# Performance work log

Measured on AMD Instinct MI355X. Metric: run time of the kernel, lower is better.

Reference implementation:

```python
import jax, jax.numpy as jnp
import numpy as np
from jax import lax

WS = 8  # window size

def conv1x1(x, W, b=None):
    y = jnp.einsum('bchw,oc->bohw', x, W)
    if b is not None:
        y = y + b[None, :, None, None]
    return y

def conv2d(x, W, b=None, dilation=1, groups=1):
    p = dilation * (W.shape[-1] // 2)
    y = lax.conv_general_dilated(x, W, (1, 1), [(p, p), (p, p)],
                                 rhs_dilation=(dilation, dilation),
                                 feature_group_count=groups,
                                 dimension_numbers=('NCHW', 'OIHW', 'NCHW'))
    if b is not None:
        y = y + b[None, :, None, None]
    return y

def ln_cf(x, w, b, eps=1e-6):
    # channels_first LayerNorm over channel dim
    u = x.mean(1, keepdims=True)
    s = ((x - u) ** 2).mean(1, keepdims=True)
    return w[None, :, None, None] * ((x - u) / jnp.sqrt(s + eps)) + b[None, :, None, None]

def to_windows(x):
    # b c (h dh) (w dw) -> b (h w) (dh dw c)
    B, C, H, W = x.shape
    h, w = H // WS, W // WS
    return x.reshape(B, C, h, WS, w, WS).transpose(0, 2, 4, 3, 5, 1).reshape(B, h * w, WS * WS * C)

def from_windows(x, C, H, W):
    B = x.shape[0]
    h, w = H // WS, W // WS
    return x.reshape(B, h, w, WS, WS, C).transpose(0, 5, 1, 3, 2, 4).reshape(B, C, H, W)

def lrelu(x):
    return jnp.where(x >= 0, x, 0.1 * x)

def gelu(x):
    return jax.nn.gelu(x, approximate=False)  # torch exact GELU

def _forward(x, w_norm1, b_norm1, w_norm2, b_norm2,
             Wv, bv, Wq, bq, Wk, bk, dw1, dwb1, dw2, dwb2, Wo, bo,
             W_in, b_in, Wc, bc, ln_w, ln_b, Wm1, bm1, Wm2, bm2,
             Wca, bca, Wsa, bsa, Wffn_in, dw_ffn, Wffn_out):
    B, C, H, W = x.shape
    ws2 = WS * WS
    N = (H // WS) * (W // WS)
    embed = ws2 * C
    # ---------- CAMixer ----------
    v = conv1x1(x, Wv, bv)
    # MaskPre routing
    xin = lrelu(conv1x1(v, W_in, b_in))                 # (B, C/4, H, W)
    x_ = lrelu(ln_cf(conv1x1(v, Wc, bc), ln_w, ln_b))   # (B, C/4, H, W)
    ca = jax.nn.sigmoid(conv1x1(x_.mean((2, 3), keepdims=True), Wca, bca))  # (B,C,1,1)
    sa = jax.nn.sigmoid(conv2d(x_, Wsa, bsa))           # (B,1,H,W)
    xm = to_windows(xin.mean(1, keepdims=True))         # (B,N,ws2)
    var = jnp.var(xm, axis=-1, ddof=1)                  # (B,N) torch.var unbiased
    k_top = N // 2
    _, idx = lax.top_k(-var, k_top)                     # bottom-k variance windows
    mbin = jnp.ones((B, N), x.dtype).at[jnp.arange(B)[:, None], idx].set(0.0)
    mfeat = jnp.broadcast_to(mbin[:, :, None], (B, N, embed))
    mask = lrelu(mfeat @ Wm1.T + bm1) @ Wm2.T + bm2     # (B,N,embed)
    # windowed content-routed attention
    vs = v * sa
    v_w, vs_w, x_w = to_windows(v), to_windows(vs), to_windows(x)
    v1 = (v_w * mask).reshape(B * N, ws2, C)
    v2 = vs_w * (1.0 - mask)
    t = (x_w * mask).reshape(B * N, ws2, C)             # masked q/k tokens (q=k=x)
    q1 = t @ Wq.T + bq
    k1 = t @ Wk.T + bk
    attn = jax.nn.softmax(q1 @ k1.transpose(0, 2, 1), axis=-1)  # (B*N, ws2, ws2)
    f = (attn @ v1).reshape(B, N, embed)
    img = from_windows(f + v2, C, H, W)
    cs = conv2d(conv2d(img, dw1, dwb1, 1, C), dw2, dwb2, 2, C)  # depthwise 3x3 + dilated
    out = gelu(cs) * ca + img
    res = conv1x1(out, Wo, bo)
    # ---------- norm1 + gated FFN + norm2 ----------
    x = ln_cf(x + res, w_norm1, b_norm1)
    y = conv2d(conv1x1(x, Wffn_in), dw_ffn, None, 1, 2 * C)
    y1, y2 = jnp.split(y, 2, axis=1)
    res = conv1x1(gelu(y1) * y2, Wffn_out)
    return ln_cf(x + res, w_norm2, b_norm2)

def setup_inputs():
    key = jax.random.key(0)
    B, C, H, W = 4, 64, 256, 256
    embed = WS * WS * C
    ks = iter(jax.random.split(key, 40))
    r = lambda *s: jax.random.normal(next(ks), s, jnp.float32) * 0.1
    return dict(
        x=jax.random.normal(next(ks), (B, C, H, W), jnp.float32),
        w_norm1=jnp.ones((C,), jnp.float32), b_norm1=jnp.zeros((C,), jnp.float32),
        w_norm2=jnp.ones((C,), jnp.float32), b_norm2=jnp.zeros((C,), jnp.float32),
        Wv=r(C, C), bv=r(C), Wq=r(C, C), bq=r(C), Wk=r(C, C), bk=r(C),
        dw1=r(C, 1, 3, 3), dwb1=r(C), dw2=r(C, 1, 3, 3), dwb2=r(C),
        Wo=r(C, C), bo=r(C),
        W_in=r(C // 4, C), b_in=r(C // 4), Wc=r(C // 4, C), bc=r(C // 4),
        ln_w=jnp.ones((C // 4,), jnp.float32), ln_b=jnp.zeros((C // 4,), jnp.float32),
        Wm1=r(embed // 2, embed) * 0.2, bm1=r(embed // 2),
        Wm2=r(embed, embed // 2) * 0.2, bm2=r(embed),
        Wca=r(C, C // 4), bca=r(C), Wsa=r(1, C // 4, 3, 3), bsa=r(1),
        Wffn_in=r(2 * C, C), dw_ffn=r(2 * C, 1, 3, 3), Wffn_out=r(C, C),
    )

def reference(x, w_norm1, b_norm1, w_norm2, b_norm2,
              Wv, bv, Wq, bq, Wk, bk, dw1, dwb1, dw2, dwb2, Wo, bo,
              W_in, b_in, Wc, bc, ln_w, ln_b, Wm1, bm1, Wm2, bm2,
              Wca, bca, Wsa, bsa, Wffn_in, dw_ffn, Wffn_out):
    return _forward(x, w_norm1, b_norm1, w_norm2, b_norm2,
                    Wv, bv, Wq, bq, Wk, bk, dw1, dwb1, dw2, dwb2, Wo, bo,
                    W_in, b_in, Wc, bc, ln_w, ln_b, Wm1, bm1, Wm2, bm2,
                    Wca, bca, Wsa, bsa, Wffn_in, dw_ffn, Wffn_out)
```

## Files before the change

### kernel.cpp

```cpp
#include <hip/hip_runtime.h>
#include <hip/hip_bf16.h>

typedef __hip_bfloat16 bf16;
typedef __attribute__((ext_vector_type(8))) short short8v;
typedef __attribute__((ext_vector_type(4))) float f32x4;

#define DEV static __device__ __forceinline__

DEV float b2f(bf16 h){ return __bfloat162float(h); }
DEV float us2f(unsigned short u){ unsigned v=((unsigned)u)<<16; float f; __builtin_memcpy(&f,&v,4); return f; }
DEV short f2bs(float f){ bf16 h=__float2bfloat16(f); short s; __builtin_memcpy(&s,&h,2); return s; }
DEV unsigned pack2(float a, float b){ return ((unsigned)(unsigned short)f2bs(b)<<16)|(unsigned short)f2bs(a); }
DEV float lrelu(float x){ return x >= 0.f ? x : 0.1f*x; }
DEV float geluf(float x){ return 0.5f*x*(1.f + erff(x*0.70710678118654752440f)); }
DEV float sigmoidf(float x){ return 1.f/(1.f + expf(-x)); }


__global__ __launch_bounds__(256) void k_detect(const void* x, int* flag){
  __shared__ int cnt;
  if(threadIdx.x==0) cnt=0;
  __syncthreads();
  const unsigned short* up=(const unsigned short*)x;
  int c=0;
  for(int k=0;k<16;k++){
    unsigned short u=up[(threadIdx.x*16+k)*2];
    if(((u>>7)&0xFF)==0xFF) c++;
  }
  atomicAdd(&cnt,c);
  __syncthreads();
  if(threadIdx.x==0) flag[0] = (cnt>0) ? 1 : 0;
}

struct CvtArgs { const void* src[31]; int sz[31]; int off[31]; };
__global__ __launch_bounds__(256) void k_cvt(CvtArgs a, const int* fl, float* wbuf){
  int t=blockIdx.x; int n=a.sz[t]; const void* s=a.src[t]; float* d=wbuf+a.off[t];
  if(fl[0]){
    const float* sp=(const float*)s;
    for(int i=threadIdx.x;i<n;i+=256) d[i]=sp[i];
  } else {
    const bf16* sp=(const bf16*)s;
    for(int i=threadIdx.x;i<n;i+=256) d[i]=b2f(sp[i]);
  }
}

__global__ __launch_bounds__(256) void k_w2b6(const float* __restrict__ wq, const float* __restrict__ wk,
    const float* __restrict__ wo, const float* __restrict__ wfi, const float* __restrict__ wfo,
    const float* __restrict__ wv,
    short* __restrict__ Wqb, short* __restrict__ Wkb,
    short* __restrict__ Wob, short* __restrict__ Wfib, short* __restrict__ Wfob,
    short* __restrict__ Wvb){
  int i=blockIdx.x*256+threadIdx.x;
  if(i<4096){ Wqb[i]=f2bs(wq[i]); Wkb[i]=f2bs(wk[i]); Wob[i]=f2bs(wo[i]); Wfob[i]=f2bs(wfo[i]); Wvb[i]=f2bs(wv[i]); }
  if(i<8192) Wfib[i]=f2bs(wfi[i]);
}

__global__ __launch_bounds__(256) void k_wcomp(const float* __restrict__ W_in, const float* __restrict__ b_in,
    const float* __restrict__ Wc, const float* __restrict__ bc,
    const float* __restrict__ Wv, const float* __restrict__ bv,
    float* __restrict__ Wa, float* __restrict__ ba,
    float* __restrict__ Wb2, float* __restrict__ bb2){
  int t=threadIdx.x;
  #pragma unroll
  for(int ii=0;ii<4;ii++){
    int idx=t+ii*256;
    int i=idx>>6, c=idx&63;
    float sa=0.f, sb=0.f;
    for(int k=0;k<64;k++){
      float wv=Wv[k*64+c];
      sa+=W_in[i*64+k]*wv;
      sb+=Wc[i*64+k]*wv;
    }
    Wa[idx]=sa; Wb2[idx]=sb;
  }
  if(t<16){
    float sa=0.f, sb=0.f;
    for(int k=0;k<64;k++){ sa+=W_in[t*64+k]*bv[k]; sb+=Wc[t*64+k]*bv[k]; }
    ba[t]=sa+b_in[t]; bb2[t]=sb+bc[t];
  }
}

__global__ __launch_bounds__(256) void k_convv_mf(
    const void* __restrict__ in, const int* __restrict__ fl,
    const short* __restrict__ Wvb, const float* __restrict__ bv,
    unsigned short* __restrict__ vw){
  __shared__ short Ain[64*72];
  int tid=threadIdx.x;
  int g0=blockIdx.x*64; int b=g0>>16, p0=g0&65535;
  int c=tid>>2, q=tid&3;
  size_t base=(((size_t)(b*64+c))<<16) + p0;
  if(fl[0]){
    const float* ip=(const float*)in + base;
    #pragma unroll
    for(int j=0;j<4;j++){
      int po=q*16+j*4;
      float4 xv=*(const float4*)(ip+po);
      Ain[(po+0)*72+c]=f2bs(xv.x); Ain[(po+1)*72+c]=f2bs(xv.y);
      Ain[(po+2)*72+c]=f2bs(xv.z); Ain[(po+3)*72+c]=f2bs(xv.w);
    }
  } else {
    const unsigned short* ip=(const unsigned short*)in + base;
    #pragma unroll
    for(int j=0;j<4;j++){
      int po=q*16+j*4;
      uint2 u=*(const uint2*)(ip+po);
      Ain[(po+0)*72+c]=(short)(u.x&0xffff); Ain[(po+1)*72+c]=(short)(u.x>>16);
      Ain[(po+2)*72+c]=(short)(u.y&0xffff); Ain[(po+3)*72+c]=(short)(u.y>>16);
    }
  }
  __syncthreads();
  int lane=tid&63, wid=tid>>6;
  int lr=lane&15, lg=lane>>4;
  int pix0=wid*16;
  short8v bfrag[2];
  #pragma unroll
  for(int ks=0;ks<2;ks++) bfrag[ks]=*(const short8v*)&Ain[(pix0+lr)*72 + ks*32 + lg*8];
  int y=p0>>8;
  int xx=(p0&255)+pix0+lr;
  int n=((y>>3)<<5)|(xx>>3), tok=((y&7)<<3)|(xx&7);
  unsigned short* wp=vw + (((size_t)(b*1024+n))<<12) + tok;
  #pragma unroll
  for(int nt=0;nt<4;nt++){
    f32x4 acc;
    #pragma unroll
    for(int r=0;r<4;r++) acc[r]=bv[nt*16+lg*4+r];
    #pragma unroll
    for(int ks=0;ks<2;ks++){
      short8v afrag=*(const short8v*)(Wvb + (nt*16+lr)*64 + ks*32 + lg*8);
      acc=__builtin_amdgcn_mfma_f32_16x16x32_bf16(afrag,bfrag[ks],acc,0,0,0);
    }
    #pragma unroll
    for(int r=0;r<4;r++){
      int m=nt*16+lg*4+r;
      wp[(size_t)m*64]=(unsigned short)f2bs(acc[r]);
    }
  }
}

__global__ __launch_bounds__(256) void k_gemm_mf(
    const void* __restrict__ in, int in_f32,
    const short* __restrict__ Wb, const float* __restrict__ bias, int has_bias,
    void* __restrict__ out, int och, int out_bf16){
  __shared__ short Ain[64*72];
  int tid=threadIdx.x;
  int g0=blockIdx.x*64; int b=g0>>16, p0=g0&65535;
  int c=tid>>2, q=tid&3;
  size_t base=(((size_t)(b*64+c))<<16) + p0;
  if(in_f32){
    const float* ip=(const float*)in + base;
    #pragma unroll
    for(int j=0;j<4;j++){
      int po=q*16+j*4;
      float4 xv=*(const float4*)(ip+po);
      Ain[(po+0)*72+c]=f2bs(xv.x); Ain[(po+1)*72+c]=f2bs(xv.y);
      Ain[(po+2)*72+c]=f2bs(xv.z); Ain[(po+3)*72+c]=f2bs(xv.w);
    }
  } else {
    const unsigned short* ip=(const unsigned short*)in + base;
    #pragma unroll
    for(int j=0;j<4;j++){
      int po=q*16+j*4;
      uint2 u=*(const uint2*)(ip+po);
      Ain[(po+0)*72+c]=(short)(u.x&0xffff); Ain[(po+1)*72+c]=(short)(u.x>>16);
      Ain[(po+2)*72+c]=(short)(u.y&0xffff); Ain[(po+3)*72+c]=(short)(u.y>>16);
    }
  }
  __syncthreads();
  int lane=tid&63, wid=tid>>6;
  int lr=lane&15, lg=lane>>4;
  int pix0=wid*16;
  short8v bfrag[2];
  #pragma unroll
  for(int ks=0;ks<2;ks++) bfrag[ks]=*(const short8v*)&Ain[(pix0+lr)*72 + ks*32 + lg*8];
  int ntn=och>>4;
  for(int nt=0;nt<ntn;nt++){
    f32x4 acc;
    if(has_bias){
      #pragma unroll
      for(int r=0;r<4;r++) acc[r]=bias[nt*16+lg*4+r];
    } else {
      acc=(f32x4){0.f,0.f,0.f,0.f};
    }
    #pragma unroll
    for(int ks=0;ks<2;ks++){
      short8v afrag=*(const short8v*)(Wb + (nt*16+lr)*64 + ks*32 + lg*8);
      acc=__builtin_amdgcn_mfma_f32_16x16x32_bf16(afrag,bfrag[ks],acc,0,0,0);
    }
    if(out_bf16){
      unsigned short* op=(unsigned short*)out;
      #pragma unroll
      for(int r=0;r<4;r++){
        int m=nt*16+lg*4+r;
        op[(((size_t)(b*och+m))<<16) + p0 + pix0 + lr]=(unsigned short)f2bs(acc[r]);
      }
    } else {
      float* op=(float*)out;
      #pragma unroll
      for(int r=0;r<4;r++){
        int m=nt*16+lg*4+r;
        op[(((size_t)(b*och+m))<<16) + p0 + pix0 + lr]=acc[r];
      }
    }
  }
}

__global__ __launch_bounds__(256) void k_gemm_ln(
    const unsigned short* __restrict__ in,
    const short* __restrict__ Wb, const float* __restrict__ bias, int has_bias,
    const void* __restrict__ basex,
    const float* __restrict__ lnw, const float* __restrict__ lnb,
    void* __restrict__ out,
    const int* __restrict__ fl, int base_mode, int out_mode){
  __shared__ short Ain[64*72];
  int tid=threadIdx.x;
  int g0=blockIdx.x*64; int b=g0>>16, p0=g0&65535;
  int c=tid>>2, q=tid&3;
  {
    const unsigned short* ip=in + (((size_t)(b*64+c))<<16) + p0;
    #pragma unroll
    for(int j=0;j<4;j++){
      int po=q*16+j*4;
      uint2 u=*(const uint2*)(ip+po);
      Ain[(po+0)*72+c]=(short)(u.x&0xffff); Ain[(po+1)*72+c]=(short)(u.x>>16);
      Ain[(po+2)*72+c]=(short)(u.y&0xffff); Ain[(po+3)*72+c]=(short)(u.y>>16);
    }
  }
  __syncthreads();
  int lane=tid&63, wid=tid>>6;
  int lr=lane&15, lg=lane>>4;
  int pix0=wid*16;
  short8v bfrag[2];
  #pragma unroll
  for(int ks=0;ks<2;ks++) bfrag[ks]=*(const short8v*)&Ain[(pix0+lr)*72 + ks*32 + lg*8];
  float rl[16];
  #pragma unroll
  for(int nt=0;nt<4;nt++){
    f32x4 acc;
    if(has_bias){
      #pragma unroll
      for(int r=0;r<4;r++) acc[r]=bias[nt*16+lg*4+r];
    } else {
      acc=(f32x4){0.f,0.f,0.f,0.f};
    }
    #pragma unroll
    for(int ks=0;ks<2;ks++){
      short8v afrag=*(const short8v*)(Wb + (nt*16+lr)*64 + ks*32 + lg*8);
      acc=__builtin_amdgcn_mfma_f32_16x16x32_bf16(afrag,bfrag[ks],acc,0,0,0);
    }
    #pragma unroll
    for(int r=0;r<4;r++) rl[nt*4+r]=acc[r];
  }
  int pix=p0+pix0+lr;
  bool bf32 = (base_mode==1) || (base_mode==0 && fl[0]);
  if(bf32){
    const float* xp=(const float*)basex;
    #pragma unroll
    for(int nt=0;nt<4;nt++)
      #pragma unroll
      for(int r=0;r<4;r++)
        rl[nt*4+r]+=xp[(((size_t)(b*64+nt*16+lg*4+r))<<16)+pix];
  } else {
    const unsigned short* xp=(const unsigned short*)basex;
    #pragma unroll
    for(int nt=0;nt<4;nt++)
      #pragma unroll
      for(int r=0;r<4;r++)
        rl[nt*4+r]+=us2f(xp[(((size_t)(b*64+nt*16+lg*4+r))<<16)+pix]);
  }
  float s=0.f;
  #pragma unroll
  for(int i=0;i<16;i++) s+=rl[i];
  s+=__shfl_xor(s,16); s+=__shfl_xor(s,32);
  float mean=s*(1.f/64.f);
  float qv=0.f;
  #pragma unroll
  for(int i=0;i<16;i++){ float d=rl[i]-mean; qv+=d*d; }
  qv+=__shfl_xor(qv,16); qv+=__shfl_xor(qv,32);
  float inv=1.f/sqrtf(qv*(1.f/64.f)+1e-6f);
  bool of32 = (out_mode==1) || (out_mode==0 && fl[0]);
  if(of32){
    float* op=(float*)out;
    #pragma unroll
    for(int nt=0;nt<4;nt++)
      #pragma unroll
      for(int r=0;r<4;r++){
        int m=nt*16+lg*4+r;
        op[(((size_t)(b*64+m))<<16)+pix]=lnw[m]*((rl[nt*4+r]-mean)*inv)+lnb[m];
      }
  } else {
    unsigned short* op=(unsigned short*)out;
    #pragma unroll
    for(int nt=0;nt<4;nt++)
      #pragma unroll
      for(int r=0;r<4;r++){
        int m=nt*16+lg*4+r;
        op[(((size_t)(b*64+m))<<16)+pix]=(unsigned short)f2bs(lnw[m]*((rl[nt*4+r]-mean)*inv)+lnb[m]);
      }
  }
}

__global__ __launch_bounds__(256) void k_route(const void* __restrict__ x, const int* __restrict__ fl,
    const float* __restrict__ Wa, const float* __restrict__ ba,
    const float* __restrict__ Wb2, const float* __restrict__ bb2,
    const float* __restrict__ lnw, const float* __restrict__ lnb,
    float* __restrict__ x_, float* __restrict__ xm, float* __restrict__ capart){
  __shared__ float wA[1024], wB[1024], sba[16], sbb[16], slw[16], slb[16];
  __shared__ float sred[4][16];
  int tid=threadIdx.x;
  for(int i=tid;i<1024;i+=256){ wA[i]=Wa[i]; wB[i]=Wb2[i]; }
  if(tid<16){ sba[tid]=ba[tid]; sbb[tid]=bb2[tid]; slw[tid]=lnw[tid]; slb[tid]=lnb[tid]; }
  __syncthreads();
  int g=blockIdx.x*512+tid*2; int b=g>>16, p=g&65535;
  float2 aA[16], aB[16];
  #pragma unroll
  for(int i=0;i<16;i++){ aA[i]=make_float2(sba[i],sba[i]); aB[i]=make_float2(sbb[i],sbb[i]); }
  size_t base=(((size_t)b*64)<<16)+p;
  if(fl[0]){
    const float* vp=(const float*)x+base;
    for(int c=0;c<64;c++){
      float2 vv=*(const float2*)(vp+(((size_t)c)<<16));
      #pragma unroll
      for(int i=0;i<16;i++){
        float wa=wA[(i<<6)+c], wb=wB[(i<<6)+c];
        aA[i].x+=wa*vv.x; aA[i].y+=wa*vv.y;
        aB[i].x+=wb*vv.x; aB[i].y+=wb*vv.y;
      }
    }
  } else {
    const unsigned short* vp=(const unsigned short*)x+base;
    for(int c=0;c<64;c++){
      unsigned u=*(const unsigned*)(vp+(((size_t)c)<<16));
      float v0=us2f(u&0xffff), v1=us2f(u>>16);
      #pragma unroll
      for(int i=0;i<16;i++){
        float wa=wA[(i<<6)+c], wb=wB[(i<<6)+c];
        aA[i].x+=wa*v0; aA[i].y+=wa*v1;
        aB[i].x+=wb*v0; aB[i].y+=wb*v1;
      }
    }
  }
  float s0=0.f,s1=0.f;
  #pragma unroll
  for(int i=0;i<16;i++){ aA[i].x=lrelu(aA[i].x); aA[i].y=lrelu(aA[i].y); s0+=aA[i].x; s1+=aA[i].y; }
  float2 xmst; xmst.x=s0*(1.f/16.f); xmst.y=s1*(1.f/16.f);
  *(float2*)(xm+g)=xmst;
  float u0=0.f,u1=0.f;
  #pragma unroll
  for(int i=0;i<16;i++){ u0+=aB[i].x; u1+=aB[i].y; }
  u0*=(1.f/16.f); u1*=(1.f/16.f);
  float q0=0.f,q1=0.f;
  #pragma unroll
  for(int i=0;i<16;i++){ float d0=aB[i].x-u0, d1=aB[i].y-u1; q0+=d0*d0; q1+=d1*d1; }
  q0*=(1.f/16.f); q1*=(1.f/16.f);
  float i0=1.f/sqrtf(q0+1e-6f), i1=1.f/sqrtf(q1+1e-6f);
  float red[16];
  float* xp=x_+(((size_t)b*16)<<16)+p;
  #pragma unroll
  for(int i=0;i<16;i++){
    float xv0=lrelu(slw[i]*((aB[i].x-u0)*i0)+slb[i]);
    float xv1=lrelu(slw[i]*((aB[i].y-u1)*i1)+slb[i]);
    float2 st; st.x=xv0; st.y=xv1;
    *(float2*)(xp+(((size_t)i)<<16))=st;
    red[i]=xv0+xv1;
  }
  int lane=tid&63, wid=tid>>6;
  #pragma unroll
  for(int i=0;i<16;i++){
    float val=red[i];
    for(int m=32;m>0;m>>=1) val+=__shfl_xor(val,m);
    if(lane==0) sred[wid][i]=val;
  }
  __syncthreads();
  if(tid<16) capart[blockIdx.x*16+tid]=sred[0][tid]+sred[1][tid]+sred[2][tid]+sred[3][tid];
}

__global__ __launch_bounds__(256) void k_sa(const float* __restrict__ x_,
    const float* __restrict__ Wsa, const float* __restrict__ bsa, unsigned short* __restrict__ sa_w){
  __shared__ float w[144]; __shared__ float bb;
  int tid=threadIdx.x;
  if(tid<144) w[tid]=Wsa[tid];
  if(tid==0) bb=bsa[0];
  __syncthreads();
  int pix=blockIdx.x*256+tid; int b=pix>>16, p=pix&65535;
  int y=p>>8, xx=p&255;
  float acc=bb;
  #pragma unroll
  for(int i=0;i<16;i++){
    const float* pl=x_+(((size_t)(b*16+i))<<16);
    #pragma unroll
    for(int ky=0;ky<3;ky++){
      int yy=y+ky-1;
      if((unsigned)yy<256u){
        #pragma unroll
        for(int kx=0;kx<3;kx++){
          int x2=xx+kx-1;
          if((unsigned)x2<256u) acc+=pl[(yy<<8)+x2]*w[i*9+ky*3+kx];
        }
      }
    }
  }
  int n=((y>>3)<<5)|(xx>>3), tok=((y&7)<<3)|(xx&7);
  sa_w[(((size_t)(b<<10)+n)<<6)+tok]=(unsigned short)f2bs(sigmoidf(acc));
}

__global__ __launch_bounds__(64) void k_var(const float* __restrict__ xm, float* __restrict__ var){
  int blk=blockIdx.x, tid=threadIdx.x;
  int b=blk>>10, n=blk&1023;
  int pix=((n>>5)<<11) + ((n&31)<<3) + ((tid>>3)<<8) + (tid&7);
  float val=xm[(b<<16)+pix];
  float s=val;
  for(int m=32;m>0;m>>=1) s+=__shfl_xor(s,m);
  float mean=s*(1.f/64.f);
  float d=val-mean; float q=d*d;
  for(int m=32;m>0;m>>=1) q+=__shfl_xor(q,m);
  if(tid==0) var[blk]=q*(1.f/63.f);
}

__global__ __launch_bounds__(256) void k_rank(const float* __restrict__ var, float* __restrict__ mbin){
  __shared__ float va[1024];
  int bid=blockIdx.x; int b=bid>>2, seg=bid&3;
  int tid=threadIdx.x;
  for(int i=tid;i<1024;i+=256) va[i]=var[(b<<10)+i];
  __syncthreads();
  int n=seg*256+tid;
  float vn=va[n]; int r=0;
  for(int m=0;m<1024;m++){ float vm=va[m]; r += (vm<vn) || (vm==vn && m<n); }
  mbin[(b<<10)+n] = (r<512)?0.f:1.f;
}

__global__ __launch_bounds__(64) void k_hvec(const void* __restrict__ Wm1, const float* __restrict__ bm1,
    float* __restrict__ h0, float* __restrict__ h1, const int* __restrict__ fl){
  int j=blockIdx.x, tid=threadIdx.x;
  float s=0.f;
  if(fl[0]){
    const float* row=(const float*)Wm1+((size_t)j<<12);
    for(int k=tid;k<4096;k+=64) s+=row[k];
  } else {
    const bf16* row=(const bf16*)Wm1+((size_t)j<<12);
    for(int k=tid;k<4096;k+=64) s+=b2f(row[k]);
  }
  for(int m=32;m>0;m>>=1) s+=__shfl_xor(s,m);
  if(tid==0){ float bb=bm1[j]; h0[j]=lrelu(bb); h1[j]=lrelu(bb+s); }
}

__global__ __launch_bounds__(64) void k_mask(const void* __restrict__ Wm2, const float* __restrict__ bm2,
    const float* __restrict__ h0, const float* __restrict__ h1,
    float* __restrict__ m0, float* __restrict__ m1,
    float* __restrict__ m0T, float* __restrict__ m1T, const int* __restrict__ fl){
  int e=blockIdx.x, tid=threadIdx.x;
  float p0=0.f,p1=0.f;
  if(fl[0]){
    const float* row=(const float*)Wm2+((size_t)e<<11);
    for(int j=tid;j<2048;j+=64){ float w=row[j]; p0+=w*h0[j]; p1+=w*h1[j]; }
  } else {
    const bf16* row=(const bf16*)Wm2+((size_t)e<<11);
    for(int j=tid;j<2048;j+=64){ float w=b2f(row[j]); p0+=w*h0[j]; p1+=w*h1[j]; }
  }
  for(int m=32;m>0;m>>=1){ p0+=__shfl_xor(p0,m); p1+=__shfl_xor(p1,m); }
  if(tid==0){
    float bb=bm2[e]; float v0=p0+bb, v1=p1+bb;
    m0[e]=v0; m1[e]=v1;
    int te=(e&63)*64+(e>>6);
    m0T[te]=v0; m1T[te]=v1;
  }
}

__global__ __launch_bounds__(64) void k_ca(const float* __restrict__ capart,
    const float* __restrict__ Wca, const float* __restrict__ bca, float* __restrict__ ca){
  __shared__ float m[16];
  int b=blockIdx.x, tid=threadIdx.x;
  if(tid<16){
    float s=0.f;
    for(int blk=0;blk<128;blk++) s+=capart[((b*128)+blk)*16+tid];
    m[tid]=s*(1.f/65536.f);
  }
  __syncthreads();
  float a=bca[tid];
  #pragma unroll
  for(int i=0;i<16;i++) a+=Wca[(tid<<4)+i]*m[i];
  ca[(b<<6)+tid]=sigmoidf(a);
}

__global__ __launch_bounds__(256) void k_pack_x(const void* __restrict__ x,
    const float* __restrict__ mbin, const float* __restrict__ m0T, const float* __restrict__ m1T,
    const int* __restrict__ fl, unsigned short* __restrict__ xwb){
  int wp=blockIdx.x; int b=wp>>9, np=wp&511;
  int n0=np*2;
  int base=((n0>>5)<<11)+((n0&31)<<3);
  int t=threadIdx.x; int c0=t>>3, row=t&7;
  int isf32=fl[0];
  const float* mTa = (mbin[b*1024+n0  ]>0.5f)? m1T : m0T;
  const float* mTb = (mbin[b*1024+n0+1]>0.5f)? m1T : m0T;
  for(int h=0;h<2;h++){
    int ch=c0+h*32;
    size_t gb=(((size_t)(b*64+ch))<<16) + base + row*256;
    float xv[16];
    if(isf32){
      const float* xp=(const float*)x+gb;
      #pragma unroll
      for(int i=0;i<16;i++) xv[i]=xp[i];
    } else {
      const bf16* xp=(const bf16*)x+gb;
      #pragma unroll
      for(int i=0;i<16;i++) xv[i]=b2f(xp[i]);
    }
    size_t o0=((size_t)(b*1024+n0)*64+ch)*64 + row*8;
    #pragma unroll
    for(int wnd=0;wnd<2;wnd++){
      const float* mT = wnd? mTb : mTa;
      size_t oo=o0+(size_t)wnd*4096;
      int s=wnd*8;
      float mk[8];
      #pragma unroll
      for(int j=0;j<8;j++) mk[j]=mT[ch*64+row*8+j];
      uint4 ux;
      ux.x=pack2(xv[s+0]*mk[0],xv[s+1]*mk[1]); ux.y=pack2(xv[s+2]*mk[2],xv[s+3]*mk[3]);
      ux.z=pack2(xv[s+4]*mk[4],xv[s+5]*mk[5]); ux.w=pack2(xv[s+6]*mk[6],xv[s+7]*mk[7]);
      *(uint4*)(xwb+oo)=ux;
    }
  }
}

#define STR 72
#define STRF 65
__global__ __launch_bounds__(256,4) void k_attn_mfma(
    const unsigned short* __restrict__ xwb, const unsigned short* __restrict__ vw,
    const unsigned short* __restrict__ sa_w, const float* __restrict__ mbin,
    const float* __restrict__ m0T, const float* __restrict__ m1T,
    const short* __restrict__ Wqb, const float* __restrict__ bq,
    const short* __restrict__ Wkb, const float* __restrict__ bk,
    unsigned short* __restrict__ img){
  __shared__ short sT[64*STR];
  __shared__ short sQK[2*64*STR];
  __shared__ short sV1[64*STR];
  __shared__ float ssa[64];
  short* sQ=sQK; short* sK=sQK+64*STR;
  float* sF=(float*)sQK;
  int tid=threadIdx.x, blk=blockIdx.x;
  int b=blk>>10, n=blk&1023;
  int base=((n>>5)<<11) + ((n&31)<<3);
  size_t plane=((size_t)b*64)<<16;
  const float* mT = (mbin[blk]>0.5f)? m1T : m0T;
  const unsigned short* xw=xwb+(size_t)blk*4096;
  const unsigned short* vw2=vw+(size_t)blk*4096;
  if(tid<64) ssa[tid]=us2f(sa_w[((size_t)blk<<6)+tid]);
  for(int e=tid;e<4096;e+=256){
    int c=e>>6, tok=e&63;
    sT[tok*STR+c]=(short)xw[e];
    sV1[c*STR+tok]=f2bs(us2f(vw2[e])*mT[e]);
  }
  __syncthreads();
  int lane=tid&63, wid=tid>>6;
  int pb=wid*16, lr=lane&15, lg=lane>>4;
  short8v ta[2];
  #pragma unroll
  for(int ks=0;ks<2;ks++) ta[ks]=*(const short8v*)&sT[(pb+lr)*STR + ks*32 + lg*8];
  #pragma unroll
  for(int nt=0;nt<4;nt++){
    float bqv=bq[nt*16+lr], bkv=bk[nt*16+lr];
    f32x4 qa={bqv,bqv,bqv,bqv}, ka={bkv,bkv,bkv,bkv};
    #pragma unroll
    for(int ks=0;ks<2;ks++){
      short8v wq=*(const short8v*)(Wqb + (nt*16+lr)*64 + ks*32 + lg*8);
      short8v wk=*(const short8v*)(Wkb + (nt*16+lr)*64 + ks*32 + lg*8);
      qa=__builtin_amdgcn_mfma_f32_16x16x32_bf16(ta[ks],wq,qa,0,0,0);
      ka=__builtin_amdgcn_mfma_f32_16x16x32_bf16(ta[ks],wk,ka,0,0,0);
    }
    #pragma unroll
    for(int r=0;r<4;r++){
      sQ[(pb+lg*4+r)*STR + nt*16+lr]=f2bs(qa[r]);
      sK[(pb+lg*4+r)*STR + nt*16+lr]=f2bs(ka[r]);
    }
  }
  __syncthreads();
  short8v qa2[2];
  #pragma unroll
  for(int ks=0;ks<2;ks++) qa2[ks]=*(const short8v*)&sQ[(pb+lr)*STR + ks*32 + lg*8];
  f32x4 sacc[4];
  #pragma unroll
  for(int nt=0;nt<4;nt++){
    f32x4 a={0.f,0.f,0.f,0.f};
    #pragma unroll
    for(int ks=0;ks<2;ks++){
      short8v kb=*(const short8v*)&sK[(nt*16+lr)*STR + ks*32 + lg*8];
      a=__builtin_amdgcn_mfma_f32_16x16x32_bf16(qa2[ks],kb,a,0,0,0);
    }
    sacc[nt]=a;
  }
  f32x4 pa[4];
  #pragma unroll
  for(int r=0;r<4;r++){
    float mx=fmaxf(fmaxf(sacc[0][r],sacc[1][r]),fmaxf(sacc[2][r],sacc[3][r]));
    #pragma unroll
    for(int m=1;m<16;m<<=1) mx=fmaxf(mx,__shfl_xor(mx,m));
    float e0=__expf(sacc[0][r]-mx), e1=__expf(sacc[1][r]-mx);
    float e2=__expf(sacc[2][r]-mx), e3=__expf(sacc[3][r]-mx);
    float sum=e0+e1+e2+e3;
    #pragma unroll
    for(int m=1;m<16;m<<=1) sum+=__shfl_xor(sum,m);
    float inv=1.f/sum;
    pa[0][r]=e0*inv; pa[1][r]=e1*inv; pa[2][r]=e2*inv; pa[3][r]=e3*inv;
  }
  #pragma unroll
  for(int nt=0;nt<4;nt++){
    #pragma unroll
    for(int r=0;r<4;r++)
      sT[(pb+lg*4+r)*STR + nt*16+lr]=f2bs(pa[nt][r]);
  }
  __syncthreads();
  short8v aa[2];
  #pragma unroll
  for(int ks=0;ks<2;ks++) aa[ks]=*(const short8v*)&sT[(pb+lr)*STR + ks*32 + lg*8];
  #pragma unroll
  for(int nt=0;nt<4;nt++){
    f32x4 f={0.f,0.f,0.f,0.f};
    #pragma unroll
    for(int ks=0;ks<2;ks++){
      short8v vb=*(const short8v*)&sV1[(nt*16+lr)*STR + ks*32 + lg*8];
      f=__builtin_amdgcn_mfma_f32_16x16x32_bf16(aa[ks],vb,f,0,0,0);
    }
    #pragma unroll
    for(int r=0;r<4;r++) sF[(pb+lg*4+r)*STRF + nt*16+lr]=f[r];
  }
  __syncthreads();
  for(int e2=tid;e2<2048;e2+=256){
    int c=e2>>5, tp=e2&31; int tok=tp*2;
    float f0=sF[tok*STRF+c], f1=sF[(tok+1)*STRF+c];
    unsigned uv=*(const unsigned*)(vw2 + c*64 + tok);
    float mk0=mT[c*64+tok], mk1=mT[c*64+tok+1];
    float vs0=us2f(uv&0xffff)*ssa[tok]*(1.f-mk0);
    float vs1=us2f(uv>>16)*ssa[tok+1]*(1.f-mk1);
    int pix=base+((tok>>3)<<8)+(tok&7);
    *(unsigned*)(img+plane+(((size_t)c)<<16)+pix)=pack2(f0+vs0, f1+vs1);
  }
}

#define DWI 264
__global__ __launch_bounds__(256) void k_dwfuse(const unsigned short* __restrict__ img,
    const float* __restrict__ dw1w, const float* __restrict__ dwb1,
    const float* __restrict__ dw2w, const float* __restrict__ dwb2,
    const float* __restrict__ ca, unsigned short* __restrict__ outb){
  __shared__ float sImg[22*DWI];
  __shared__ float sTmp[20*DWI];
  __shared__ float k1[9], k2[9];
  __shared__ float bb1, bb2, cav;
  int bid=blockIdx.x; int b=bid>>10, c=(bid>>4)&63, sy=bid&15;
  int y0=sy*16;
  int tid=threadIdx.x;
  if(tid<9){ k1[tid]=dw1w[c*9+tid]; k2[tid]=dw2w[c*9+tid]; }
  if(tid==9)  bb1=dwb1[c];
  if(tid==10) bb2=dwb2[c];
  if(tid==11) cav=ca[b*64+c];
  const unsigned short* ip=img+(((size_t)(b*64+c))<<16);
  for(int task=tid;task<1452;task+=256){
    int r=task/66, j=task-r*66;
    int gy=y0-3+r, gx0=4*j-4;
    float4 v=make_float4(0.f,0.f,0.f,0.f);
    if((unsigned)gy<256u && j>=1 && j<=64){
      uint2 u=*(const uint2*)(ip+(gy<<8)+gx0);
      v.x=us2f(u.x&0xffff); v.y=us2f(u.x>>16); v.z=us2f(u.y&0xffff); v.w=us2f(u.y>>16);
    }
    *(float4*)&sImg[r*DWI+4*j]=v;
  }
  __syncthreads();
  for(int task=tid;task<1300;task+=256){
    int r=task/65, g=task-r*65;
    int ty=y0-2+r, tc0=4*g-2;
    float t[4]={bb1,bb1,bb1,bb1};
    #pragma unroll
    for(int dy=0;dy<3;dy++){
      float4 A0=*(const float4*)&sImg[(r+dy)*DWI+4*g];
      float4 A1=*(const float4*)&sImg[(r+dy)*DWI+4*g+4];
      float F[8]={A0.x,A0.y,A0.z,A0.w,A1.x,A1.y,A1.z,A1.w};
      #pragma unroll
      for(int dx=0;dx<3;dx++){
        float kk=k1[dy*3+dx];
        #pragma unroll
        for(int e=0;e<4;e++) t[e]+=F[1+e+dx]*kk;
      }
    }
    float4 res;
    bool rowok=((unsigned)ty<256u);
    #pragma unroll
    for(int e=0;e<4;e++){
      int tc=tc0+e;
      ((float*)&res)[e]= (rowok && (unsigned)tc<256u)? t[e] : 0.f;
    }
    *(float4*)&sTmp[r*DWI+4*g]=res;
  }
  __syncthreads();
  int q=tid&63, rr=tid>>6;
  unsigned short* op=outb+(((size_t)(b*64+c))<<16);
  #pragma unroll
  for(int l4=0;l4<4;l4++){
    int ly=rr*4+l4;
    float cs[4]={bb2,bb2,bb2,bb2};
    #pragma unroll
    for(int dy=0;dy<3;dy++){
      int r=ly+2*dy;
      float4 T0=*(const float4*)&sTmp[r*DWI+4*q];
      float4 T1=*(const float4*)&sTmp[r*DWI+4*q+4];
      float T[8]={T0.x,T0.y,T0.z,T0.w,T1.x,T1.y,T1.z,T1.w};
      #pragma unroll
      for(int dx=0;dx<3;dx++){
        float kk=k2[dy*3+dx];
        #pragma unroll
        for(int e=0;e<4;e++) cs[e]+=T[e+2*dx]*kk;
      }
    }
    float4 C=*(const float4*)&sImg[(ly+3)*DWI+4*q+4];
    float o0=geluf(cs[0])*cav+C.x;
    float o1=geluf(cs[1])*cav+C.y;
    float o2=geluf(cs[2])*cav+C.z;
    float o3=geluf(cs[3])*cav+C.w;
    uint2 u; u.x=pack2(o0,o1); u.y=pack2(o2,o3);
    *(uint2*)(op+((y0+ly)<<8)+4*q)=u;
  }
}

#define FEI 264
__global__ __launch_bounds__(256) void k_ffn_dw_t(const unsigned short* __restrict__ E,
    const float* __restrict__ dwf, unsigned short* __restrict__ g){
  __shared__ unsigned short sE1[18*FEI];
  __shared__ unsigned short sE2[18*FEI];
  __shared__ float k1[9], k2[9];
  int bid=blockIdx.x; int b=bid>>10, c=(bid>>4)&63, sy=bid&15;
  int y0=sy*16;
  int tid=threadIdx.x;
  if(tid<9){ k1[tid]=dwf[c*9+tid]; k2[tid]=dwf[(64+c)*9+tid]; }
  const unsigned short* p1=E+(((size_t)(b*128+c))<<16);
  const unsigned short* p2=E+(((size_t)(b*128+64+c))<<16);
  for(int task=tid;task<1188;task+=256){
    int r=task/66, j=task-r*66;
    int gy=y0-1+r, gx0=4*j-4;
    uint2 u1=make_uint2(0,0), u2=make_uint2(0,0);
    if((unsigned)gy<256u && j>=1 && j<=64){
      u1=*(const uint2*)(p1+(gy<<8)+gx0);
      u2=*(const uint2*)(p2+(gy<<8)+gx0);
    }
    *(uint2*)&sE1[r*FEI+4*j]=u1;
    *(uint2*)&sE2[r*FEI+4*j]=u2;
  }
  __syncthreads();
  int q=tid&63, rr=tid>>6;
  unsigned short* op=g+(((size_t)(b*64+c))<<16);
  #pragma unroll
  for(int l4=0;l4<4;l4++){
    int ly=rr*4+l4;
    float a1[4]={0.f,0.f,0.f,0.f}, a2[4]={0.f,0.f,0.f,0.f};
    #pragma unroll
    for(int dy=0;dy<3;dy++){
      int r=ly+dy;
      unsigned w0=*(const unsigned*)&sE1[r*FEI+4*q+2];
      uint2   w1=*(const uint2*)  &sE1[r*FEI+4*q+4];
      unsigned w2=*(const unsigned*)&sE1[r*FEI+4*q+8];
      float GA[6]={us2f(w0>>16),us2f(w1.x&0xffff),us2f(w1.x>>16),us2f(w1.y&0xffff),us2f(w1.y>>16),us2f(w2&0xffff)};
      unsigned v0=*(const unsigned*)&sE2[r*FEI+4*q+2];
      uint2   v1=*(const uint2*)  &sE2[r*FEI+4*q+4];
      unsigned v2=*(const unsigned*)&sE2[r*FEI+4*q+8];
      float GB[6]={us2f(v0>>16),us2f(v1.x&0xffff),us2f(v1.x>>16),us2f(v1.y&0xffff),us2f(v1.y>>16),us2f(v2&0xffff)};
      #pragma unroll
      for(int dx=0;dx<3;dx++){
        float ka=k1[dy*3+dx], kb=k2[dy*3+dx];
        #pragma unroll
        for(int e=0;e<4;e++){
          a1[e]+=GA[e+dx]*ka;
          a2[e]+=GB[e+dx]*kb;
        }
      }
    }
    float o0=geluf(a1[0])*a2[0];
    float o1=geluf(a1[1])*a2[1];
    float o2=geluf(a1[2])*a2[2];
    float o3=geluf(a1[3])*a2[3];
    uint2 u; u.x=pack2(o0,o1); u.y=pack2(o2,o3);
    *(uint2*)(op+((y0+ly)<<8)+4*q)=u;
  }
}

extern "C" void kernel_launch(void* const* d_in, const int* in_sizes, int n_in,
                              void* d_out, int out_size, void* d_ws, size_t ws_size,
                              hipStream_t stream){
  (void)in_sizes; (void)n_in; (void)out_size; (void)ws_size;
  const void* x  = d_in[0];
  const void* Wm1= d_in[23];
  const void* Wm2= d_in[25];

  char* ws=(char*)d_ws;
  unsigned short* E=(unsigned short*)(ws);
  unsigned short* img=(unsigned short*)(ws+67108864);
  unsigned short* x1b=(unsigned short*)(ws+67108864);
  unsigned short* xwb=(unsigned short*)(ws+134217728);
  unsigned short* outb=(unsigned short*)(ws+134217728);
  unsigned short* gbuf=(unsigned short*)(ws+134217728);
  unsigned short* vw =(unsigned short*)(ws+230686720);
  char* sm = ws+201326592;
  float* x_    =(float*)(sm);
  unsigned short* sa_w=(unsigned short*)(sm+16777216);
  float* xm    =(float*)(sm+17825792);
  float* var   =(float*)(sm+18874368);
  float* mbin  =(float*)(sm+18890752);
  float* h0    =(float*)(sm+18907136);
  float* h1    =(float*)(sm+18915328);
  float* m0    =(float*)(sm+18923520);
  float* m1    =(float*)(sm+18939904);
  float* capart=(float*)(sm+18956288);
  float* ca    =(float*)(sm+19021824);
  int*   flag  =(int*)  (sm+19022848);
  float* wbuf  =(float*)(sm+19023872);
  short* Wqb   =(short*)(sm+19200000);
  short* Wkb   =(short*)(sm+19208192);
  float* m0T   =(float*)(sm+19216384);
  float* m1T   =(float*)(sm+19232768);
  short* Wob   =(short*)(sm+19249152);
  short* Wfib  =(short*)(sm+19257344);
  short* Wfob  =(short*)(sm+19273728);
  short* Wvb   =(short*)(sm+19281920);
  float* WaC   =(float*)(sm+19290112);
  float* WbC   =(float*)(sm+19294208);
  float* baC   =(float*)(sm+19298304);
  float* bbC   =(float*)(sm+19298560);

  static const int din_idx[31]={5,6,7,8,9,10,11,12,13,14,15,16,17,18,19,20,21,22,24,26,27,28,29,30,31,32,33,1,2,3,4};
  static const int szs[31]  ={4096,64,4096,64,4096,64,576,64,576,64,4096,64,1024,16,1024,16,16,16,2048,4096,1024,64,144,1,8192,1152,4096,64,64,64,64};
  CvtArgs ca_args;
  int off=0;
  int offs[31];
  for(int t=0;t<31;t++){
    ca_args.src[t]=d_in[din_idx[t]];
    ca_args.sz[t]=szs[t];
    ca_args.off[t]=off;
    offs[t]=off;
    off+=szs[t];
  }
  const float* Wv  =wbuf+offs[0];  const float* bv  =wbuf+offs[1];
  const float* Wq  =wbuf+offs[2];  const float* bq  =wbuf+offs[3];
  const float* Wk  =wbuf+offs[4];  const float* bk  =wbuf+offs[5];
  const float* dw1 =wbuf+offs[6];  const float* dwb1=wbuf+offs[7];
  const float* dw2 =wbuf+offs[8];  const float* dwb2=wbuf+offs[9];
  const float* Wo  =wbuf+offs[10]; const float* bo  =wbuf+offs[11];
  const float* W_in=wbuf+offs[12]; const float* b_in=wbuf+offs[13];
  const float* Wc  =wbuf+offs[14]; const float* bc  =wbuf+offs[15];
  const float* lnw =wbuf+offs[16]; const float* lnb =wbuf+offs[17];
  const float* bm1 =wbuf+offs[18]; const float* bm2 =wbuf+offs[19];
  const float* Wca =wbuf+offs[20]; const float* bca =wbuf+offs[21];
  const float* Wsa =wbuf+offs[22]; const float* bsa =wbuf+offs[23];
  const float* Wfi =wbuf+offs[24]; const float* dwf =wbuf+offs[25];
  const float* Wfo =wbuf+offs[26];
  const float* wn1 =wbuf+offs[27]; const float* bn1 =wbuf+offs[28];
  const float* wn2 =wbuf+offs[29]; const float* bn2 =wbuf+offs[30];

  hipLaunchKernelGGL(k_detect,   dim3(1),      dim3(256), 0, stream, x, flag);
  hipLaunchKernelGGL(k_cvt,      dim3(31),     dim3(256), 0, stream, ca_args, flag, wbuf);
  hipLaunchKernelGGL(k_w2b6,     dim3(32),     dim3(256), 0, stream, Wq, Wk, Wo, Wfi, Wfo, Wv, Wqb, Wkb, Wob, Wfib, Wfob, Wvb);
  hipLaunchKernelGGL(k_wcomp,    dim3(1),      dim3(256), 0, stream, W_in, b_in, Wc, bc, Wv, bv, WaC, baC, WbC, bbC);
  hipLaunchKernelGGL(k_convv_mf, dim3(4096),   dim3(256), 0, stream, x, flag, Wvb, bv, vw);
  hipLaunchKernelGGL(k_route,    dim3(512),    dim3(256), 0, stream, x, flag, WaC, baC, WbC, bbC, lnw, lnb, x_, xm, capart);
  hipLaunchKernelGGL(k_sa,       dim3(1024),   dim3(256), 0, stream, x_, Wsa, bsa, sa_w);
  hipLaunchKernelGGL(k_var,      dim3(4096),   dim3(64),  0, stream, xm, var);
  hipLaunchKernelGGL(k_rank,     dim3(16),     dim3(256), 0, stream, var, mbin);
  hipLaunchKernelGGL(k_hvec,     dim3(2048),   dim3(64),  0, stream, Wm1, bm1, h0, h1, flag);
  hipLaunchKernelGGL(k_mask,     dim3(4096),   dim3(64),  0, stream, Wm2, bm2, h0, h1, m0, m1, m0T, m1T, flag);
  hipLaunchKernelGGL(k_ca,       dim3(4),      dim3(64),  0, stream, capart, Wca, bca, ca);
  hipLaunchKernelGGL(k_pack_x,   dim3(2048),   dim3(256), 0, stream, x, mbin, m0T, m1T, flag, xwb);
  hipLaunchKernelGGL(k_attn_mfma,dim3(4096),   dim3(256), 0, stream, xwb, vw, sa_w, mbin, m0T, m1T, Wqb, bq, Wkb, bk, img);
  hipLaunchKernelGGL(k_dwfuse,   dim3(4096),   dim3(256), 0, stream, img, dw1, dwb1, dw2, dwb2, ca, outb);
  hipLaunchKernelGGL(k_gemm_ln,  dim3(4096),   dim3(256), 0, stream, outb, Wob, bo, 1, x, wn1, bn1, (void*)x1b, flag, 0, 2);
  hipLaunchKernelGGL(k_gemm_mf,  dim3(4096),   dim3(256), 0, stream, (const void*)x1b, 0, Wfib, wbuf, 0, (void*)E, 128, 1);
  hipLaunchKernelGGL(k_ffn_dw_t, dim3(4096),   dim3(256), 0, stream, E, dwf, gbuf);
  hipLaunchKernelGGL(k_gemm_ln,  dim3(4096),   dim3(256), 0, stream, gbuf, Wfob, wbuf, 0, (const void*)x1b, wn2, bn2, d_out, flag, 2, 0);
}
```

Before: 505.1 us.

## Store packed windows token-major and read MFMA operands directly from global

k_pack_x now stages each pair of masked windows in shared memory and writes them token-major (token x channel) with coalesced 16-byte stores. This lets k_attn_mfma load its Q/K MFMA A-operand straight from global memory and drop the sT transpose buffer. The V staging loop is vectorized to 16-byte loads and stores. The softmax probabilities reuse the sQ region, and one barrier is removed by reading them back within the same wave before syncing. The launch_bounds occupancy hint is dropped, which adds a risk of different register allocation, and the pack kernel gains shared-memory traffic and a barrier.

```diff
diff --git a/kernel.cpp b/kernel.cpp
--- a/kernel.cpp
+++ b/kernel.cpp
@@ -483,15 +483,16 @@
 __global__ __launch_bounds__(256) void k_pack_x(const void* __restrict__ x,
     const float* __restrict__ mbin, const float* __restrict__ m0T, const float* __restrict__ m1T,
     const int* __restrict__ fl, unsigned short* __restrict__ xwb){
+  __shared__ unsigned short sW[2*64*72];
   int wp=blockIdx.x; int b=wp>>9, np=wp&511;
   int n0=np*2;
   int base=((n0>>5)<<11)+((n0&31)<<3);
-  int t=threadIdx.x; int c0=t>>3, row=t&7;
+  int t=threadIdx.x; int ch0=t&31, row=t>>5;
   int isf32=fl[0];
   const float* mTa = (mbin[b*1024+n0  ]>0.5f)? m1T : m0T;
   const float* mTb = (mbin[b*1024+n0+1]>0.5f)? m1T : m0T;
   for(int h=0;h<2;h++){
-    int ch=c0+h*32;
+    int ch=ch0+h*32;
     size_t gb=(((size_t)(b*64+ch))<<16) + base + row*256;
     float xv[16];
     if(isf32){
@@ -503,33 +504,36 @@
       #pragma unroll
       for(int i=0;i<16;i++) xv[i]=b2f(xp[i]);
     }
-    size_t o0=((size_t)(b*1024+n0)*64+ch)*64 + row*8;
     #pragma unroll
     for(int wnd=0;wnd<2;wnd++){
       const float* mT = wnd? mTb : mTa;
-      size_t oo=o0+(size_t)wnd*4096;
       int s=wnd*8;
-      float mk[8];
-      #pragma unroll
-      for(int j=0;j<8;j++) mk[j]=mT[ch*64+row*8+j];
-      uint4 ux;
-      ux.x=pack2(xv[s+0]*mk[0],xv[s+1]*mk[1]); ux.y=pack2(xv[s+2]*mk[2],xv[s+3]*mk[3]);
-      ux.z=pack2(xv[s+4]*mk[4],xv[s+5]*mk[5]); ux.w=pack2(xv[s+6]*mk[6],xv[s+7]*mk[7]);
-      *(uint4*)(xwb+oo)=ux;
-    }
+      #pragma unroll
+      for(int j=0;j<8;j++){
+        float mk=mT[ch*64+row*8+j];
+        sW[wnd*4608 + (row*8+j)*72 + ch]=(unsigned short)f2bs(xv[s+j]*mk);
+      }
+    }
+  }
+  __syncthreads();
+  size_t ob=((size_t)(b*1024+n0))<<12;
+  #pragma unroll
+  for(int k2=0;k2<4;k2++){
+    int idx=t+k2*256; int win=idx>>9, rem=idx&511, tok=rem>>3, cg=rem&7;
+    uint4 val=*(const uint4*)&sW[win*4608 + tok*72 + cg*8];
+    *(uint4*)(xwb + ob + (size_t)win*4096 + tok*64 + cg*8)=val;
   }
 }
 
 #define STR 72
 #define STRF 65
-__global__ __launch_bounds__(256,4) void k_attn_mfma(
+__global__ __launch_bounds__(256) void k_attn_mfma(
     const unsigned short* __restrict__ xwb, const unsigned short* __restrict__ vw,
     const unsigned short* __restrict__ sa_w, const float* __restrict__ mbin,
     const float* __restrict__ m0T, const float* __restrict__ m1T,
     const short* __restrict__ Wqb, const float* __restrict__ bq,
     const short* __restrict__ Wkb, const float* __restrict__ bk,
     unsigned short* __restrict__ img){
-  __shared__ short sT[64*STR];
   __shared__ short sQK[2*64*STR];
   __shared__ short sV1[64*STR];
   __shared__ float ssa[64];
@@ -543,17 +547,23 @@
   const unsigned short* xw=xwb+(size_t)blk*4096;
   const unsigned short* vw2=vw+(size_t)blk*4096;
   if(tid<64) ssa[tid]=us2f(sa_w[((size_t)blk<<6)+tid]);
-  for(int e=tid;e<4096;e+=256){
-    int c=e>>6, tok=e&63;
-    sT[tok*STR+c]=(short)xw[e];
-    sV1[c*STR+tok]=f2bs(us2f(vw2[e])*mT[e]);
-  }
-  __syncthreads();
+  for(int task=tid;task<512;task+=256){
+    int c=task>>3, tok0=(task&7)*8;
+    uint4 uv=*(const uint4*)(vw2 + c*64 + tok0);
+    float4 ma=*(const float4*)(mT + c*64 + tok0);
+    float4 mb=*(const float4*)(mT + c*64 + tok0 + 4);
+    uint4 o;
+    o.x=pack2(us2f(uv.x&0xffff)*ma.x, us2f(uv.x>>16)*ma.y);
+    o.y=pack2(us2f(uv.y&0xffff)*ma.z, us2f(uv.y>>16)*ma.w);
+    o.z=pack2(us2f(uv.z&0xffff)*mb.x, us2f(uv.z>>16)*mb.y);
+    o.w=pack2(us2f(uv.w&0xffff)*mb.z, us2f(uv.w>>16)*mb.w);
+    *(uint4*)&sV1[c*STR+tok0]=o;
+  }
   int lane=tid&63, wid=tid>>6;
   int pb=wid*16, lr=lane&15, lg=lane>>4;
   short8v ta[2];
   #pragma unroll
-  for(int ks=0;ks<2;ks++) ta[ks]=*(const short8v*)&sT[(pb+lr)*STR + ks*32 + lg*8];
+  for(int ks=0;ks<2;ks++) ta[ks]=*(const short8v*)(xw + (pb+lr)*64 + ks*32 + lg*8);
   #pragma unroll
   for(int nt=0;nt<4;nt++){
     float bqv=bq[nt*16+lr], bkv=bk[nt*16+lr];
@@ -604,12 +614,12 @@
   for(int nt=0;nt<4;nt++){
     #pragma unroll
     for(int r=0;r<4;r++)
-      sT[(pb+lg*4+r)*STR + nt*16+lr]=f2bs(pa[nt][r]);
-  }
-  __syncthreads();
+      sQ[(pb+lg*4+r)*STR + nt*16+lr]=f2bs(pa[nt][r]);
+  }
   short8v aa[2];
   #pragma unroll
-  for(int ks=0;ks<2;ks++) aa[ks]=*(const short8v*)&sT[(pb+lr)*STR + ks*32 + lg*8];
+  for(int ks=0;ks<2;ks++) aa[ks]=*(const short8v*)&sQ[(pb+lr)*STR + ks*32 + lg*8];
+  __syncthreads();
   #pragma unroll
   for(int nt=0;nt<4;nt++){
     f32x4 f={0.f,0.f,0.f,0.f};
```

Result: no change. 508.3 us (+0.6%).
